# Performance work log

Measured on AMD Instinct MI355X. Metric: run time of the kernel, lower is better.

Reference implementation:

```python
import jax, jax.numpy as jnp
import numpy as np
import math

D_MODEL = 512
NUM_HEADS = 8
D_HEAD = D_MODEL // NUM_HEADS
B, S = 8, 1024


def _rel_shift(pos_score):
    # pos_score: [B, H, S, S] -> Transformer-XL relative shift
    b, h, s1, s2 = pos_score.shape
    padded = jnp.concatenate([jnp.zeros((b, h, s1, 1), pos_score.dtype), pos_score], axis=-1)
    padded = padded.reshape(b, h, s2 + 1, s1)
    return padded[:, :, 1:].reshape(b, h, s1, s2)


def setup_inputs() -> dict:
    key = jax.random.key(0)
    ks = jax.random.split(key, 16)
    scale = 1.0 / math.sqrt(D_MODEL)
    inp = {
        'query': jax.random.normal(ks[0], (B, S, D_MODEL), jnp.float32),
        'key': jax.random.normal(ks[1], (B, S, D_MODEL), jnp.float32),
        'value': jax.random.normal(ks[2], (B, S, D_MODEL), jnp.float32),
        'position_emb': jax.random.normal(ks[3], (B, S, D_MODEL), jnp.float32),
        'Wq': jax.random.normal(ks[4], (D_MODEL, D_MODEL), jnp.float32) * scale,
        'bq': jnp.zeros((D_MODEL,), jnp.float32),
        'Wk': jax.random.normal(ks[5], (D_MODEL, D_MODEL), jnp.float32) * scale,
        'bk': jnp.zeros((D_MODEL,), jnp.float32),
        'Wv': jax.random.normal(ks[6], (D_MODEL, D_MODEL), jnp.float32) * scale,
        'bv': jnp.zeros((D_MODEL,), jnp.float32),
        'Wp': jax.random.normal(ks[7], (D_MODEL, D_MODEL), jnp.float32) * scale,
        'u_bias': jax.random.normal(ks[8], (NUM_HEADS, D_HEAD), jnp.float32) * 0.1,
        'v_bias': jax.random.normal(ks[9], (NUM_HEADS, D_HEAD), jnp.float32) * 0.1,
        'Wo': jax.random.normal(ks[10], (D_MODEL, D_MODEL), jnp.float32) * scale,
        'bo': jnp.zeros((D_MODEL,), jnp.float32),
    }
    return inp


def reference(query, key, value, position_emb, Wq, bq, Wk, bk, Wv, bv, Wp, u_bias, v_bias, Wo, bo):
    b, s, _ = query.shape
    q = (query @ Wq + bq).reshape(b, s, NUM_HEADS, D_HEAD)       # [B,S,H,Dh]
    k = (key @ Wk + bk).reshape(b, s, NUM_HEADS, D_HEAD)
    v = (value @ Wv + bv).reshape(b, s, NUM_HEADS, D_HEAD)
    p = (position_emb @ Wp).reshape(b, s, NUM_HEADS, D_HEAD)
    # content score: (q + u) k^T ; pos score: (q + v) p^T with relative shift
    content_score = jnp.einsum('bqhd,bkhd->bhqk', q + u_bias, k)
    pos_score = _rel_shift(jnp.einsum('bqhd,bkhd->bhqk', q + v_bias, p))
    score = (content_score + pos_score) / math.sqrt(D_MODEL)
    atten = jax.nn.softmax(score, axis=-1)                        # dropout off (eval)
    context = jnp.einsum('bhqk,bkhd->bqhd', atten, v).reshape(b, s, D_MODEL)
    return context @ Wo + bo
```

## Files before the change

kernel.cpp:

```cpp
#include <hip/hip_runtime.h>
#include <cstdint>

typedef unsigned short ushort_t;
typedef __attribute__((ext_vector_type(8))) short bf16x8;
typedef __attribute__((ext_vector_type(4))) float f32x4;

#define S_LEN 1024
#define DHEAD 64

__device__ inline ushort_t f2bf(float f) {
    union { float f; uint32_t u; } c; c.f = f;
    uint32_t u = c.u;
    uint32_t r = u + 0x7FFFu + ((u >> 16) & 1u);
    return (ushort_t)(r >> 16);
}
__device__ inline float bf2f(ushort_t h) {
    union { uint32_t u; float f; } c; c.u = ((uint32_t)h) << 16;
    return c.f;
}
__device__ inline bf16x8 load8(const ushort_t* p) {
    union { uint4 u; bf16x8 v; } c;
    c.u = *reinterpret_cast<const uint4*>(p);
    return c.v;
}

__global__ void prep_kernel(const float* __restrict__ wq, const float* __restrict__ wk,
                            const float* __restrict__ wv, const float* __restrict__ wp,
                            const float* __restrict__ wo, ushort_t* __restrict__ ws) {
    int t = blockIdx.x * 256 + threadIdx.x;
    int wi = blockIdx.y;
    const float* src = wi == 0 ? wq : wi == 1 ? wk : wi == 2 ? wv : wi == 3 ? wp : wo;
    int r = t >> 9, c = t & 511;
    ws[(size_t)wi * 262144 + (size_t)c * 512 + r] = f2bf(src[t]);
}

__global__ __launch_bounds__(256) void proj_gemm(
    const float* __restrict__ qa, const float* __restrict__ ka,
    const float* __restrict__ va, const float* __restrict__ pa,
    const ushort_t* __restrict__ wT,
    const float* __restrict__ bq, const float* __restrict__ bk,
    const float* __restrict__ bv,
    const float* __restrict__ ub, const float* __restrict__ vb,
    ushort_t* __restrict__ Qu, ushort_t* __restrict__ Qv,
    ushort_t* __restrict__ Kp, ushort_t* __restrict__ Pp,
    ushort_t* __restrict__ Vt) {
    __shared__ ushort_t As[128][72];
    __shared__ ushort_t Bs[128][72];
    int z = blockIdx.z;
    const float* A = z == 0 ? qa : z == 1 ? ka : z == 2 ? pa : va;
    const ushort_t* Bt = wT + (z == 0 ? 0 : z == 1 ? 262144 : z == 2 ? 786432 : 524288);
    const float* bias = z == 0 ? bq : z == 1 ? bk : z == 3 ? bv : nullptr;

    int tid = threadIdx.x;
    int wid = tid >> 6, lane = tid & 63, quad = lane >> 4, l16 = lane & 15;
    int wr = wid >> 1, wc = wid & 1;
    int row0 = blockIdx.y * 128, col0 = blockIdx.x * 128;

    f32x4 acc[4][4];
#pragma unroll
    for (int i = 0; i < 4; i++)
#pragma unroll
        for (int j = 0; j < 4; j++) acc[i][j] = (f32x4){0.f, 0.f, 0.f, 0.f};

    for (int k0 = 0; k0 < 512; k0 += 64) {
#pragma unroll
        for (int i = 0; i < 4; i++) {
            int cid = tid + i * 256;
            int r = cid >> 3, c8 = cid & 7;
            const float* ap = A + (size_t)(row0 + r) * 512 + k0 + c8 * 8;
            float4 f0 = *reinterpret_cast<const float4*>(ap);
            float4 f1 = *reinterpret_cast<const float4*>(ap + 4);
            union { ushort_t s[8]; uint4 u; } pk;
            pk.s[0] = f2bf(f0.x); pk.s[1] = f2bf(f0.y); pk.s[2] = f2bf(f0.z); pk.s[3] = f2bf(f0.w);
            pk.s[4] = f2bf(f1.x); pk.s[5] = f2bf(f1.y); pk.s[6] = f2bf(f1.z); pk.s[7] = f2bf(f1.w);
            *reinterpret_cast<uint4*>(&As[r][c8 * 8]) = pk.u;
            *reinterpret_cast<uint4*>(&Bs[r][c8 * 8]) =
                *reinterpret_cast<const uint4*>(Bt + (size_t)(col0 + r) * 512 + k0 + c8 * 8);
        }
        __syncthreads();
#pragma unroll
        for (int kc = 0; kc < 2; kc++) {
            bf16x8 af[4], bg[4];
#pragma unroll
            for (int m = 0; m < 4; m++)
                af[m] = load8(&As[wr * 64 + m * 16 + l16][kc * 32 + quad * 8]);
#pragma unroll
            for (int n = 0; n < 4; n++)
                bg[n] = load8(&Bs[wc * 64 + n * 16 + l16][kc * 32 + quad * 8]);
#pragma unroll
            for (int m = 0; m < 4; m++)
#pragma unroll
                for (int n = 0; n < 4; n++)
                    acc[m][n] = __builtin_amdgcn_mfma_f32_16x16x32_bf16(af[m], bg[n], acc[m][n], 0, 0, 0);
        }
        __syncthreads();
    }

#pragma unroll
    for (int m = 0; m < 4; m++) {
#pragma unroll
        for (int n = 0; n < 4; n++) {
            int col = col0 + wc * 64 + n * 16 + l16;
            float bcol = bias ? bias[col] : 0.f;
#pragma unroll
            for (int r = 0; r < 4; r++) {
                int row = row0 + wr * 64 + m * 16 + quad * 4 + r;
                float val = acc[m][n][r] + bcol;
                int b_ = row >> 10, s_ = row & 1023, h_ = col >> 6, d_ = col & 63;
                if (z == 0) {
                    size_t idx = (((size_t)(b_ * 8 + h_)) * 1024 + s_) * 64 + d_;
                    Qu[idx] = f2bf(val + ub[col]);
                    Qv[idx] = f2bf(val + vb[col]);
                } else if (z == 3) {
                    size_t idx = (((size_t)(b_ * 8 + h_)) * 64 + d_) * 1024 + s_;
                    Vt[idx] = f2bf(val);
                } else {
                    size_t idx = (((size_t)(b_ * 8 + h_)) * 1024 + s_) * 64 + d_;
                    (z == 1 ? Kp : Pp)[idx] = f2bf(val);
                }
            }
        }
    }
}

__global__ __launch_bounds__(256) void out_gemm(
    const ushort_t* __restrict__ A, const ushort_t* __restrict__ Bt,
    const float* __restrict__ bias, float* __restrict__ outf) {
    __shared__ ushort_t As[128][72];
    __shared__ ushort_t Bs[128][72];
    int tid = threadIdx.x;
    int wid = tid >> 6, lane = tid & 63, quad = lane >> 4, l16 = lane & 15;
    int wr = wid >> 1, wc = wid & 1;
    int row0 = blockIdx.y * 128, col0 = blockIdx.x * 128;

    f32x4 acc[4][4];
#pragma unroll
    for (int i = 0; i < 4; i++)
#pragma unroll
        for (int j = 0; j < 4; j++) acc[i][j] = (f32x4){0.f, 0.f, 0.f, 0.f};

    for (int k0 = 0; k0 < 512; k0 += 64) {
#pragma unroll
        for (int i = 0; i < 4; i++) {
            int cid = tid + i * 256;
            int r = cid >> 3, c8 = cid & 7;
            *reinterpret_cast<uint4*>(&As[r][c8 * 8]) =
                *reinterpret_cast<const uint4*>(A + (size_t)(row0 + r) * 512 + k0 + c8 * 8);
            *reinterpret_cast<uint4*>(&Bs[r][c8 * 8]) =
                *reinterpret_cast<const uint4*>(Bt + (size_t)(col0 + r) * 512 + k0 + c8 * 8);
        }
        __syncthreads();
#pragma unroll
        for (int kc = 0; kc < 2; kc++) {
            bf16x8 af[4], bg[4];
#pragma unroll
            for (int m = 0; m < 4; m++)
                af[m] = load8(&As[wr * 64 + m * 16 + l16][kc * 32 + quad * 8]);
#pragma unroll
            for (int n = 0; n < 4; n++)
                bg[n] = load8(&Bs[wc * 64 + n * 16 + l16][kc * 32 + quad * 8]);
#pragma unroll
            for (int m = 0; m < 4; m++)
#pragma unroll
                for (int n = 0; n < 4; n++)
                    acc[m][n] = __builtin_amdgcn_mfma_f32_16x16x32_bf16(af[m], bg[n], acc[m][n], 0, 0, 0);
        }
        __syncthreads();
    }
#pragma unroll
    for (int m = 0; m < 4; m++)
#pragma unroll
        for (int n = 0; n < 4; n++) {
            int col = col0 + wc * 64 + n * 16 + l16;
#pragma unroll
            for (int r = 0; r < 4; r++) {
                int row = row0 + wr * 64 + m * 16 + quad * 4 + r;
                outf[(size_t)row * 512 + col] = acc[m][n][r] + bias[col];
            }
        }
}

__global__ __launch_bounds__(256) void attn_kernel(
    const ushort_t* __restrict__ Qu, const ushort_t* __restrict__ Qv,
    const ushort_t* __restrict__ Kp, const ushort_t* __restrict__ Pp,
    const ushort_t* __restrict__ Vt, ushort_t* __restrict__ ctxb) {
    __shared__ ushort_t sc[16][1032];
    __shared__ float red1[4][16];
    __shared__ float red2[4][16];

    constexpr float SCL = (float)(1.4426950408889634 / 22.627416997969522);

    int bx = blockIdx.x;
    int bh = bx >> 6, q0 = (bx & 63) << 4;
    int tid = threadIdx.x, wid = tid >> 6, lane = tid & 63;
    int quad = lane >> 4, l16 = lane & 15;

    const ushort_t* Qu_b = Qu + (size_t)bh * S_LEN * DHEAD;
    const ushort_t* Qv_b = Qv + (size_t)bh * S_LEN * DHEAD;
    const ushort_t* K_b  = Kp + (size_t)bh * S_LEN * DHEAD;
    const ushort_t* P_b  = Pp + (size_t)bh * S_LEN * DHEAD;
    const ushort_t* V_b  = Vt + (size_t)bh * DHEAD * S_LEN;

    bf16x8 au[2], av1[2], av2[2];
#pragma unroll
    for (int kc = 0; kc < 2; kc++) {
        au[kc]  = load8(Qu_b + (size_t)(q0 + l16) * 64 + kc * 32 + quad * 8);
        av1[kc] = load8(Qv_b + (size_t)(q0 + l16) * 64 + kc * 32 + quad * 8);
        int r2 = q0 + 1 + l16; if (r2 > S_LEN - 1) r2 = S_LEN - 1;
        av2[kc] = load8(Qv_b + (size_t)r2 * 64 + kc * 32 + quad * 8);
    }

    int kw0 = wid << 8, kw1 = kw0 + 256;

    if (lane < 16) {
        int kz = q0 + lane + 1;
        if (kz >= kw0 && kz < kw1) sc[lane][kz] = 0;
    }

    if (kw0 <= q0 + 15) {
        int wlo = (S_LEN - 16) - q0 + kw0;
        int d1 = kw1 - 1 - q0; if (d1 > 0) d1 = 0;
        int whi = (S_LEN - 1) + d1;
        for (int wt = wlo; wt <= whi; wt += 16) {
            int prow = wt + l16; if (prow > S_LEN - 1) prow = S_LEN - 1;
            bf16x8 b0 = load8(P_b + (size_t)prow * 64 + quad * 8);
            bf16x8 b1 = load8(P_b + (size_t)prow * 64 + 32 + quad * 8);
            f32x4 acc = (f32x4){0.f, 0.f, 0.f, 0.f};
            acc = __builtin_amdgcn_mfma_f32_16x16x32_bf16(av1[0], b0, acc, 0, 0, 0);
            acc = __builtin_amdgcn_mfma_f32_16x16x32_bf16(av1[1], b1, acc, 0, 0, 0);
#pragma unroll
            for (int r = 0; r < 4; r++) {
                int m = quad * 4 + r, q = q0 + m;
                int k = wt + l16 - (S_LEN - 1) + q;
                if (k >= kw0 && k < kw1 && k <= q) sc[m][k] = f2bf(acc[r]);
            }
        }
    }
    if (kw1 - 1 >= q0 + 2) {
        int wlo2 = kw0 - q0 - 17; if (wlo2 < 0) wlo2 = 0;
        int whi2 = kw1 - 3 - q0;
        for (int wt = wlo2; wt <= whi2; wt += 16) {
            int prow = wt + l16; if (prow > S_LEN - 1) prow = S_LEN - 1;
            bf16x8 b0 = load8(P_b + (size_t)prow * 64 + quad * 8);
            bf16x8 b1 = load8(P_b + (size_t)prow * 64 + 32 + quad * 8);
            f32x4 acc = (f32x4){0.f, 0.f, 0.f, 0.f};
            acc = __builtin_amdgcn_mfma_f32_16x16x32_bf16(av2[0], b0, acc, 0, 0, 0);
            acc = __builtin_amdgcn_mfma_f32_16x16x32_bf16(av2[1], b1, acc, 0, 0, 0);
#pragma unroll
            for (int r = 0; r < 4; r++) {
                int m = quad * 4 + r, q = q0 + m;
                int k = wt + l16 + q + 2;
                if (k >= kw0 && k < kw1) sc[m][k] = f2bf(acc[r]);
            }
        }
    }

    float pm[4] = {-1e30f, -1e30f, -1e30f, -1e30f};
    for (int nt = 0; nt < 16; ++nt) {
        int kt = kw0 + nt * 16;
        bf16x8 b0 = load8(K_b + (size_t)(kt + l16) * 64 + quad * 8);
        bf16x8 b1 = load8(K_b + (size_t)(kt + l16) * 64 + 32 + quad * 8);
        f32x4 acc;
#pragma unroll
        for (int r = 0; r < 4; r++) acc[r] = bf2f(sc[quad * 4 + r][kt + l16]);
        acc = __builtin_amdgcn_mfma_f32_16x16x32_bf16(au[0], b0, acc, 0, 0, 0);
        acc = __builtin_amdgcn_mfma_f32_16x16x32_bf16(au[1], b1, acc, 0, 0, 0);
#pragma unroll
        for (int r = 0; r < 4; r++) {
            sc[quad * 4 + r][kt + l16] = f2bf(acc[r]);
            pm[r] = fmaxf(pm[r], acc[r]);
        }
    }
#pragma unroll
    for (int off = 1; off < 16; off <<= 1)
#pragma unroll
        for (int r = 0; r < 4; r++) pm[r] = fmaxf(pm[r], __shfl_xor(pm[r], off));
    if (l16 == 0) {
#pragma unroll
        for (int r = 0; r < 4; r++) red1[wid][quad * 4 + r] = pm[r];
    }
    __syncthreads();

    int row = tid & 15, cb = tid >> 4;
    float rm = fmaxf(fmaxf(red1[0][row], red1[1][row]), fmaxf(red1[2][row], red1[3][row]));
    float ssum = 0.f;
    ushort_t* sp = &sc[row][cb * 64];
#pragma unroll
    for (int j = 0; j < 8; j++) {
        union { uint4 u; ushort_t s[8]; } in, out;
        in.u = *reinterpret_cast<uint4*>(sp + j * 8);
#pragma unroll
        for (int e = 0; e < 8; e++) {
            float ev = exp2f((bf2f(in.s[e]) - rm) * SCL);
            out.s[e] = f2bf(ev);
            ssum += ev;
        }
        *reinterpret_cast<uint4*>(sp + j * 8) = out.u;
    }
    ssum += __shfl_xor(ssum, 16);
    ssum += __shfl_xor(ssum, 32);
    if (lane < 16) red2[wid][lane] = ssum;
    __syncthreads();

    int d0 = wid << 4;
    f32x4 acc = (f32x4){0.f, 0.f, 0.f, 0.f};
    for (int kc = 0; kc < 32; ++kc) {
        bf16x8 a = load8(&sc[l16][kc * 32 + quad * 8]);
        bf16x8 b = load8(V_b + (size_t)(d0 + l16) * 1024 + kc * 32 + quad * 8);
        acc = __builtin_amdgcn_mfma_f32_16x16x32_bf16(a, b, acc, 0, 0, 0);
    }
    int b_ = bh >> 3, h_ = bh & 7;
#pragma unroll
    for (int r = 0; r < 4; r++) {
        int m = quad * 4 + r, q = q0 + m;
        float s = red2[0][m] + red2[1][m] + red2[2][m] + red2[3][m];
        ctxb[((size_t)b_ * 1024 + q) * 512 + h_ * 64 + d0 + l16] = f2bf(acc[r] / s);
    }
}

extern "C" void kernel_launch(void* const* d_in, const int* in_sizes, int n_in,
                              void* d_out, int out_size, void* d_ws, size_t ws_size,
                              hipStream_t stream) {
    const float* q  = (const float*)d_in[0];
    const float* k  = (const float*)d_in[1];
    const float* v  = (const float*)d_in[2];
    const float* pe = (const float*)d_in[3];
    const float* Wq = (const float*)d_in[4];
    const float* bq = (const float*)d_in[5];
    const float* Wk = (const float*)d_in[6];
    const float* bk = (const float*)d_in[7];
    const float* Wv = (const float*)d_in[8];
    const float* bv = (const float*)d_in[9];
    const float* Wp = (const float*)d_in[10];
    const float* ub = (const float*)d_in[11];
    const float* vbias = (const float*)d_in[12];
    const float* Wo = (const float*)d_in[13];
    const float* bo = (const float*)d_in[14];
    float* out = (float*)d_out;
    ushort_t* ws = (ushort_t*)d_ws;

    ushort_t* wT  = ws;
    ushort_t* Qu  = ws + 1310720;
    ushort_t* Qv  = Qu + 4194304;
    ushort_t* Kp  = Qv + 4194304;
    ushort_t* Pp  = Kp + 4194304;
    ushort_t* Vt  = Pp + 4194304;
    ushort_t* ctx = Vt + 4194304;

    prep_kernel<<<dim3(1024, 5), 256, 0, stream>>>(Wq, Wk, Wv, Wp, Wo, wT);
    proj_gemm<<<dim3(4, 64, 4), 256, 0, stream>>>(q, k, v, pe, wT, bq, bk, bv,
                                                  ub, vbias, Qu, Qv, Kp, Pp, Vt);
    attn_kernel<<<4096, 256, 0, stream>>>(Qu, Qv, Kp, Pp, Vt, ctx);
    out_gemm<<<dim3(4, 64), 256, 0, stream>>>(ctx, wT + 4 * 262144, bo, out);
}
```

Before: 382.6 us.

## Double query tile in attention, coalesce V transpose and weight prep, prefetch loads

The attention kernel now handles 32 query rows per block instead of 16, so each K and V tile load feeds two MFMA row tiles, and the grid shrinks to half as many blocks. K, P and V fragments are software-prefetched one iteration ahead, and the softmax normalisation uses precomputed reciprocals. Separately, the V projection epilogue stages its output through shared memory so the transposed Vt writes are coalesced, and the weight prep kernel uses a tiled shared-memory transpose. The larger score buffer (about 66KB LDS) may reduce occupancy.

```diff
diff --git a/kernel.cpp b/kernel.cpp
--- a/kernel.cpp
+++ b/kernel.cpp
@@ -24,14 +24,34 @@
     return c.v;
 }
 
-__global__ void prep_kernel(const float* __restrict__ wq, const float* __restrict__ wk,
-                            const float* __restrict__ wv, const float* __restrict__ wp,
-                            const float* __restrict__ wo, ushort_t* __restrict__ ws) {
-    int t = blockIdx.x * 256 + threadIdx.x;
-    int wi = blockIdx.y;
+__global__ __launch_bounds__(256) void prep_kernel(
+    const float* __restrict__ wq, const float* __restrict__ wk,
+    const float* __restrict__ wv, const float* __restrict__ wp,
+    const float* __restrict__ wo, ushort_t* __restrict__ ws) {
+    __shared__ float tile[64][65];
+    int wi = blockIdx.z;
     const float* src = wi == 0 ? wq : wi == 1 ? wk : wi == 2 ? wv : wi == 3 ? wp : wo;
-    int r = t >> 9, c = t & 511;
-    ws[(size_t)wi * 262144 + (size_t)c * 512 + r] = f2bf(src[t]);
+    int cx = blockIdx.x * 64;
+    int ry = blockIdx.y * 64;
+    int t = threadIdx.x;
+    int tr = t >> 4;
+    int tc = (t & 15) * 4;
+#pragma unroll
+    for (int i = 0; i < 4; i++) {
+        int r = tr + i * 16;
+        float4 f = *reinterpret_cast<const float4*>(src + (size_t)(ry + r) * 512 + cx + tc);
+        tile[r][tc] = f.x; tile[r][tc + 1] = f.y; tile[r][tc + 2] = f.z; tile[r][tc + 3] = f.w;
+    }
+    __syncthreads();
+    ushort_t* dst = ws + (size_t)wi * 262144;
+#pragma unroll
+    for (int i = 0; i < 4; i++) {
+        int r = tr + i * 16;
+        ushort4 o;
+        o.x = f2bf(tile[tc][r]); o.y = f2bf(tile[tc + 1][r]);
+        o.z = f2bf(tile[tc + 2][r]); o.w = f2bf(tile[tc + 3][r]);
+        *reinterpret_cast<ushort4*>(dst + (size_t)(cx + r) * 512 + ry + tc) = o;
+    }
 }
 
 __global__ __launch_bounds__(256) void proj_gemm(
@@ -44,8 +64,7 @@
     ushort_t* __restrict__ Qu, ushort_t* __restrict__ Qv,
     ushort_t* __restrict__ Kp, ushort_t* __restrict__ Pp,
     ushort_t* __restrict__ Vt) {
-    __shared__ ushort_t As[128][72];
-    __shared__ ushort_t Bs[128][72];
+    __shared__ ushort_t smem[2][128][72];
     int z = blockIdx.z;
     const float* A = z == 0 ? qa : z == 1 ? ka : z == 2 ? pa : va;
     const ushort_t* Bt = wT + (z == 0 ? 0 : z == 1 ? 262144 : z == 2 ? 786432 : 524288);
@@ -73,8 +92,8 @@
             union { ushort_t s[8]; uint4 u; } pk;
             pk.s[0] = f2bf(f0.x); pk.s[1] = f2bf(f0.y); pk.s[2] = f2bf(f0.z); pk.s[3] = f2bf(f0.w);
             pk.s[4] = f2bf(f1.x); pk.s[5] = f2bf(f1.y); pk.s[6] = f2bf(f1.z); pk.s[7] = f2bf(f1.w);
-            *reinterpret_cast<uint4*>(&As[r][c8 * 8]) = pk.u;
-            *reinterpret_cast<uint4*>(&Bs[r][c8 * 8]) =
+            *reinterpret_cast<uint4*>(&smem[0][r][c8 * 8]) = pk.u;
+            *reinterpret_cast<uint4*>(&smem[1][r][c8 * 8]) =
                 *reinterpret_cast<const uint4*>(Bt + (size_t)(col0 + r) * 512 + k0 + c8 * 8);
         }
         __syncthreads();
@@ -83,10 +102,10 @@
             bf16x8 af[4], bg[4];
 #pragma unroll
             for (int m = 0; m < 4; m++)
-                af[m] = load8(&As[wr * 64 + m * 16 + l16][kc * 32 + quad * 8]);
+                af[m] = load8(&smem[0][wr * 64 + m * 16 + l16][kc * 32 + quad * 8]);
 #pragma unroll
             for (int n = 0; n < 4; n++)
-                bg[n] = load8(&Bs[wc * 64 + n * 16 + l16][kc * 32 + quad * 8]);
+                bg[n] = load8(&smem[1][wc * 64 + n * 16 + l16][kc * 32 + quad * 8]);
 #pragma unroll
             for (int m = 0; m < 4; m++)
 #pragma unroll
@@ -96,30 +115,54 @@
         __syncthreads();
     }
 
-#pragma unroll
-    for (int m = 0; m < 4; m++) {
-#pragma unroll
-        for (int n = 0; n < 4; n++) {
-            int col = col0 + wc * 64 + n * 16 + l16;
-            float bcol = bias ? bias[col] : 0.f;
-#pragma unroll
-            for (int r = 0; r < 4; r++) {
-                int row = row0 + wr * 64 + m * 16 + quad * 4 + r;
-                float val = acc[m][n][r] + bcol;
-                int b_ = row >> 10, s_ = row & 1023, h_ = col >> 6, d_ = col & 63;
-                if (z == 0) {
+    if (z == 3) {
+        ushort_t (*Ts)[130] = reinterpret_cast<ushort_t(*)[130]>(&smem[0][0][0]);
+#pragma unroll
+        for (int m = 0; m < 4; m++)
+#pragma unroll
+            for (int n = 0; n < 4; n++) {
+                int dl = wc * 64 + n * 16 + l16;
+                float bcol = bv[col0 + dl];
+#pragma unroll
+                for (int r = 0; r < 4; r++) {
+                    int sl = wr * 64 + m * 16 + quad * 4 + r;
+                    Ts[dl][sl] = f2bf(acc[m][n][r] + bcol);
+                }
+            }
+        __syncthreads();
+        int b_ = row0 >> 10, s0 = row0 & 1023;
+#pragma unroll
+        for (int p = 0; p < 8; p++) {
+            int dl = p * 16 + (tid >> 4);
+            int sl = (tid & 15) * 8;
+            int col = col0 + dl, h_ = col >> 6, d_ = col & 63;
+            ushort_t* dst = Vt + (((size_t)(b_ * 8 + h_)) * 64 + d_) * 1024 + s0 + sl;
+            union { uint4 u; ushort_t s[8]; } pk;
+#pragma unroll
+            for (int e = 0; e < 8; e++) pk.s[e] = Ts[dl][sl + e];
+            *reinterpret_cast<uint4*>(dst) = pk.u;
+        }
+    } else {
+#pragma unroll
+        for (int m = 0; m < 4; m++)
+#pragma unroll
+            for (int n = 0; n < 4; n++) {
+                int col = col0 + wc * 64 + n * 16 + l16;
+                float bcol = bias ? bias[col] : 0.f;
+#pragma unroll
+                for (int r = 0; r < 4; r++) {
+                    int row = row0 + wr * 64 + m * 16 + quad * 4 + r;
+                    float val = acc[m][n][r] + bcol;
+                    int b_ = row >> 10, s_ = row & 1023, h_ = col >> 6, d_ = col & 63;
                     size_t idx = (((size_t)(b_ * 8 + h_)) * 1024 + s_) * 64 + d_;
-                    Qu[idx] = f2bf(val + ub[col]);
-                    Qv[idx] = f2bf(val + vb[col]);
-                } else if (z == 3) {
-                    size_t idx = (((size_t)(b_ * 8 + h_)) * 64 + d_) * 1024 + s_;
-                    Vt[idx] = f2bf(val);
-                } else {
-                    size_t idx = (((size_t)(b_ * 8 + h_)) * 1024 + s_) * 64 + d_;
-                    (z == 1 ? Kp : Pp)[idx] = f2bf(val);
+                    if (z == 0) {
+                        Qu[idx] = f2bf(val + ub[col]);
+                        Qv[idx] = f2bf(val + vb[col]);
+                    } else {
+                        (z == 1 ? Kp : Pp)[idx] = f2bf(val);
+                    }
                 }
             }
-        }
     }
 }
 
@@ -184,14 +227,15 @@
     const ushort_t* __restrict__ Qu, const ushort_t* __restrict__ Qv,
     const ushort_t* __restrict__ Kp, const ushort_t* __restrict__ Pp,
     const ushort_t* __restrict__ Vt, ushort_t* __restrict__ ctxb) {
-    __shared__ ushort_t sc[16][1032];
-    __shared__ float red1[4][16];
-    __shared__ float red2[4][16];
+    __shared__ ushort_t sc[32][1032];
+    __shared__ float red1[4][32];
+    __shared__ float red2[32][8];
+    __shared__ float rowinv[32];
 
     constexpr float SCL = (float)(1.4426950408889634 / 22.627416997969522);
 
     int bx = blockIdx.x;
-    int bh = bx >> 6, q0 = (bx & 63) << 4;
+    int bh = bx >> 5, q0 = (bx & 31) << 5;
     int tid = threadIdx.x, wid = tid >> 6, lane = tid & 63;
     int quad = lane >> 4, l16 = lane & 15;
 
@@ -201,92 +245,134 @@
     const ushort_t* P_b  = Pp + (size_t)bh * S_LEN * DHEAD;
     const ushort_t* V_b  = Vt + (size_t)bh * DHEAD * S_LEN;
 
-    bf16x8 au[2], av1[2], av2[2];
+    int kw0 = wid << 8, kw1 = kw0 + 256;
+
+    bf16x8 au0[2], au1[2];
 #pragma unroll
     for (int kc = 0; kc < 2; kc++) {
-        au[kc]  = load8(Qu_b + (size_t)(q0 + l16) * 64 + kc * 32 + quad * 8);
-        av1[kc] = load8(Qv_b + (size_t)(q0 + l16) * 64 + kc * 32 + quad * 8);
-        int r2 = q0 + 1 + l16; if (r2 > S_LEN - 1) r2 = S_LEN - 1;
-        av2[kc] = load8(Qv_b + (size_t)r2 * 64 + kc * 32 + quad * 8);
-    }
-
-    int kw0 = wid << 8, kw1 = kw0 + 256;
-
-    if (lane < 16) {
+        au0[kc] = load8(Qu_b + (size_t)(q0 + l16) * 64 + kc * 32 + quad * 8);
+        au1[kc] = load8(Qu_b + (size_t)(q0 + 16 + l16) * 64 + kc * 32 + quad * 8);
+    }
+
+    if (lane < 32) {
         int kz = q0 + lane + 1;
         if (kz >= kw0 && kz < kw1) sc[lane][kz] = 0;
     }
 
-    if (kw0 <= q0 + 15) {
-        int wlo = (S_LEN - 16) - q0 + kw0;
-        int d1 = kw1 - 1 - q0; if (d1 > 0) d1 = 0;
-        int whi = (S_LEN - 1) + d1;
-        for (int wt = wlo; wt <= whi; wt += 16) {
-            int prow = wt + l16; if (prow > S_LEN - 1) prow = S_LEN - 1;
-            bf16x8 b0 = load8(P_b + (size_t)prow * 64 + quad * 8);
-            bf16x8 b1 = load8(P_b + (size_t)prow * 64 + 32 + quad * 8);
-            f32x4 acc = (f32x4){0.f, 0.f, 0.f, 0.f};
-            acc = __builtin_amdgcn_mfma_f32_16x16x32_bf16(av1[0], b0, acc, 0, 0, 0);
-            acc = __builtin_amdgcn_mfma_f32_16x16x32_bf16(av1[1], b1, acc, 0, 0, 0);
-#pragma unroll
-            for (int r = 0; r < 4; r++) {
-                int m = quad * 4 + r, q = q0 + m;
-                int k = wt + l16 - (S_LEN - 1) + q;
-                if (k >= kw0 && k < kw1 && k <= q) sc[m][k] = f2bf(acc[r]);
+#pragma unroll
+    for (int mt = 0; mt < 2; mt++) {
+        int q0m = q0 + mt * 16;
+        bf16x8 av1[2], av2[2];
+#pragma unroll
+        for (int kc = 0; kc < 2; kc++) {
+            av1[kc] = load8(Qv_b + (size_t)(q0m + l16) * 64 + kc * 32 + quad * 8);
+            int r2 = q0m + 1 + l16; if (r2 > S_LEN - 1) r2 = S_LEN - 1;
+            av2[kc] = load8(Qv_b + (size_t)r2 * 64 + kc * 32 + quad * 8);
+        }
+        if (kw0 <= q0m + 15) {
+            int wlo = (S_LEN - 16) - q0m + kw0;
+            int d1 = kw1 - 1 - q0m; if (d1 > 0) d1 = 0;
+            int whi = (S_LEN - 1) + d1;
+            int pr = wlo + l16; if (pr > S_LEN - 1) pr = S_LEN - 1;
+            bf16x8 p0 = load8(P_b + (size_t)pr * 64 + quad * 8);
+            bf16x8 p1 = load8(P_b + (size_t)pr * 64 + 32 + quad * 8);
+            for (int wt = wlo; wt <= whi; wt += 16) {
+                bf16x8 b0 = p0, b1 = p1;
+                if (wt + 16 <= whi) {
+                    int pn = wt + 16 + l16; if (pn > S_LEN - 1) pn = S_LEN - 1;
+                    p0 = load8(P_b + (size_t)pn * 64 + quad * 8);
+                    p1 = load8(P_b + (size_t)pn * 64 + 32 + quad * 8);
+                }
+                f32x4 acc = (f32x4){0.f, 0.f, 0.f, 0.f};
+                acc = __builtin_amdgcn_mfma_f32_16x16x32_bf16(av1[0], b0, acc, 0, 0, 0);
+                acc = __builtin_amdgcn_mfma_f32_16x16x32_bf16(av1[1], b1, acc, 0, 0, 0);
+#pragma unroll
+                for (int r = 0; r < 4; r++) {
+                    int m = quad * 4 + r, q = q0m + m;
+                    int k = wt + l16 - (S_LEN - 1) + q;
+                    if (k >= kw0 && k < kw1 && k <= q) sc[mt * 16 + m][k] = f2bf(acc[r]);
+                }
             }
         }
-    }
-    if (kw1 - 1 >= q0 + 2) {
-        int wlo2 = kw0 - q0 - 17; if (wlo2 < 0) wlo2 = 0;
-        int whi2 = kw1 - 3 - q0;
-        for (int wt = wlo2; wt <= whi2; wt += 16) {
-            int prow = wt + l16; if (prow > S_LEN - 1) prow = S_LEN - 1;
-            bf16x8 b0 = load8(P_b + (size_t)prow * 64 + quad * 8);
-            bf16x8 b1 = load8(P_b + (size_t)prow * 64 + 32 + quad * 8);
-            f32x4 acc = (f32x4){0.f, 0.f, 0.f, 0.f};
-            acc = __builtin_amdgcn_mfma_f32_16x16x32_bf16(av2[0], b0, acc, 0, 0, 0);
-            acc = __builtin_amdgcn_mfma_f32_16x16x32_bf16(av2[1], b1, acc, 0, 0, 0);
-#pragma unroll
-            for (int r = 0; r < 4; r++) {
-                int m = quad * 4 + r, q = q0 + m;
-                int k = wt + l16 + q + 2;
-                if (k >= kw0 && k < kw1) sc[m][k] = f2bf(acc[r]);
+        if (kw1 - 1 >= q0m + 2) {
+            int wlo2 = kw0 - q0m - 17; if (wlo2 < 0) wlo2 = 0;
+            int whi2 = kw1 - 3 - q0m;
+            int pr = wlo2 + l16; if (pr > S_LEN - 1) pr = S_LEN - 1;
+            bf16x8 p0 = load8(P_b + (size_t)pr * 64 + quad * 8);
+            bf16x8 p1 = load8(P_b + (size_t)pr * 64 + 32 + quad * 8);
+            for (int wt = wlo2; wt <= whi2; wt += 16) {
+                bf16x8 b0 = p0, b1 = p1;
+                if (wt + 16 <= whi2) {
+                    int pn = wt + 16 + l16; if (pn > S_LEN - 1) pn = S_LEN - 1;
+                    p0 = load8(P_b + (size_t)pn * 64 + quad * 8);
+                    p1 = load8(P_b + (size_t)pn * 64 + 32 + quad * 8);
+                }
+                f32x4 acc = (f32x4){0.f, 0.f, 0.f, 0.f};
+                acc = __builtin_amdgcn_mfma_f32_16x16x32_bf16(av2[0], b0, acc, 0, 0, 0);
+                acc = __builtin_amdgcn_mfma_f32_16x16x32_bf16(av2[1], b1, acc, 0, 0, 0);
+#pragma unroll
+                for (int r = 0; r < 4; r++) {
+                    int m = quad * 4 + r, q = q0m + m;
+                    int k = wt + l16 + q + 2;
+                    if (k >= kw0 && k < kw1) sc[mt * 16 + m][k] = f2bf(acc[r]);
+                }
             }
         }
     }
 
-    float pm[4] = {-1e30f, -1e30f, -1e30f, -1e30f};
+    float pm0[4] = {-1e30f, -1e30f, -1e30f, -1e30f};
+    float pm1[4] = {-1e30f, -1e30f, -1e30f, -1e30f};
+    const ushort_t* Kw = K_b + (size_t)kw0 * 64;
+    bf16x8 k0 = load8(Kw + (size_t)l16 * 64 + quad * 8);
+    bf16x8 k1 = load8(Kw + (size_t)l16 * 64 + 32 + quad * 8);
     for (int nt = 0; nt < 16; ++nt) {
         int kt = kw0 + nt * 16;
-        bf16x8 b0 = load8(K_b + (size_t)(kt + l16) * 64 + quad * 8);
-        bf16x8 b1 = load8(K_b + (size_t)(kt + l16) * 64 + 32 + quad * 8);
-        f32x4 acc;
-#pragma unroll
-        for (int r = 0; r < 4; r++) acc[r] = bf2f(sc[quad * 4 + r][kt + l16]);
-        acc = __builtin_amdgcn_mfma_f32_16x16x32_bf16(au[0], b0, acc, 0, 0, 0);
-        acc = __builtin_amdgcn_mfma_f32_16x16x32_bf16(au[1], b1, acc, 0, 0, 0);
+        bf16x8 b0 = k0, b1 = k1;
+        if (nt < 15) {
+            const ushort_t* kp = Kw + (size_t)((nt + 1) * 16 + l16) * 64;
+            k0 = load8(kp + quad * 8);
+            k1 = load8(kp + 32 + quad * 8);
+        }
+        f32x4 a0, a1;
 #pragma unroll
         for (int r = 0; r < 4; r++) {
-            sc[quad * 4 + r][kt + l16] = f2bf(acc[r]);
-            pm[r] = fmaxf(pm[r], acc[r]);
+            a0[r] = bf2f(sc[quad * 4 + r][kt + l16]);
+            a1[r] = bf2f(sc[16 + quad * 4 + r][kt + l16]);
+        }
+        a0 = __builtin_amdgcn_mfma_f32_16x16x32_bf16(au0[0], b0, a0, 0, 0, 0);
+        a0 = __builtin_amdgcn_mfma_f32_16x16x32_bf16(au0[1], b1, a0, 0, 0, 0);
+        a1 = __builtin_amdgcn_mfma_f32_16x16x32_bf16(au1[0], b0, a1, 0, 0, 0);
+        a1 = __builtin_amdgcn_mfma_f32_16x16x32_bf16(au1[1], b1, a1, 0, 0, 0);
+#pragma unroll
+        for (int r = 0; r < 4; r++) {
+            sc[quad * 4 + r][kt + l16] = f2bf(a0[r]);
+            sc[16 + quad * 4 + r][kt + l16] = f2bf(a1[r]);
+            pm0[r] = fmaxf(pm0[r], a0[r]);
+            pm1[r] = fmaxf(pm1[r], a1[r]);
         }
     }
 #pragma unroll
     for (int off = 1; off < 16; off <<= 1)
 #pragma unroll
-        for (int r = 0; r < 4; r++) pm[r] = fmaxf(pm[r], __shfl_xor(pm[r], off));
+        for (int r = 0; r < 4; r++) {
+            pm0[r] = fmaxf(pm0[r], __shfl_xor(pm0[r], off));
+            pm1[r] = fmaxf(pm1[r], __shfl_xor(pm1[r], off));
+        }
     if (l16 == 0) {
 #pragma unroll
-        for (int r = 0; r < 4; r++) red1[wid][quad * 4 + r] = pm[r];
+        for (int r = 0; r < 4; r++) {
+            red1[wid][quad * 4 + r] = pm0[r];
+            red1[wid][16 + quad * 4 + r] = pm1[r];
+        }
     }
     __syncthreads();
 
-    int row = tid & 15, cb = tid >> 4;
+    int row = tid & 31, cb = tid >> 5;
     float rm = fmaxf(fmaxf(red1[0][row], red1[1][row]), fmaxf(red1[2][row], red1[3][row]));
     float ssum = 0.f;
-    ushort_t* sp = &sc[row][cb * 64];
-#pragma unroll
-    for (int j = 0; j < 8; j++) {
+    ushort_t* sp = &sc[row][cb * 128];
+#pragma unroll
+    for (int j = 0; j < 16; j++) {
         union { uint4 u; ushort_t s[8]; } in, out;
         in.u = *reinterpret_cast<uint4*>(sp + j * 8);
 #pragma unroll
@@ -297,24 +383,37 @@
         }
         *reinterpret_cast<uint4*>(sp + j * 8) = out.u;
     }
-    ssum += __shfl_xor(ssum, 16);
-    ssum += __shfl_xor(ssum, 32);
-    if (lane < 16) red2[wid][lane] = ssum;
+    red2[row][cb] = ssum;
     __syncthreads();
+    if (tid < 32) {
+        float s = 0.f;
+#pragma unroll
+        for (int c = 0; c < 8; c++) s += red2[tid][c];
+        rowinv[tid] = 1.0f / s;
+    }
 
     int d0 = wid << 4;
-    f32x4 acc = (f32x4){0.f, 0.f, 0.f, 0.f};
+    const ushort_t* Vw = V_b + (size_t)(d0 + l16) * 1024;
+    bf16x8 vb0 = load8(Vw + quad * 8);
+    f32x4 ac0 = (f32x4){0.f, 0.f, 0.f, 0.f};
+    f32x4 ac1 = (f32x4){0.f, 0.f, 0.f, 0.f};
     for (int kc = 0; kc < 32; ++kc) {
-        bf16x8 a = load8(&sc[l16][kc * 32 + quad * 8]);
-        bf16x8 b = load8(V_b + (size_t)(d0 + l16) * 1024 + kc * 32 + quad * 8);
-        acc = __builtin_amdgcn_mfma_f32_16x16x32_bf16(a, b, acc, 0, 0, 0);
-    }
+        bf16x8 b = vb0;
+        if (kc < 31) vb0 = load8(Vw + (kc + 1) * 32 + quad * 8);
+        bf16x8 a0 = load8(&sc[l16][kc * 32 + quad * 8]);
+        bf16x8 a1 = load8(&sc[16 + l16][kc * 32 + quad * 8]);
+        ac0 = __builtin_amdgcn_mfma_f32_16x16x32_bf16(a0, b, ac0, 0, 0, 0);
+        ac1 = __builtin_amdgcn_mfma_f32_16x16x32_bf16(a1, b, ac1, 0, 0, 0);
+    }
+    __syncthreads();
     int b_ = bh >> 3, h_ = bh & 7;
 #pragma unroll
     for (int r = 0; r < 4; r++) {
-        int m = quad * 4 + r, q = q0 + m;
-        float s = red2[0][m] + red2[1][m] + red2[2][m] + red2[3][m];
-        ctxb[((size_t)b_ * 1024 + q) * 512 + h_ * 64 + d0 + l16] = f2bf(acc[r] / s);
+        int m = quad * 4 + r;
+        ctxb[((size_t)b_ * 1024 + (q0 + m)) * 512 + h_ * 64 + d0 + l16] =
+            f2bf(ac0[r] * rowinv[m]);
+        ctxb[((size_t)b_ * 1024 + (q0 + 16 + m)) * 512 + h_ * 64 + d0 + l16] =
+            f2bf(ac1[r] * rowinv[16 + m]);
     }
 }
 
@@ -347,9 +446,9 @@
     ushort_t* Vt  = Pp + 4194304;
     ushort_t* ctx = Vt + 4194304;
 
-    prep_kernel<<<dim3(1024, 5), 256, 0, stream>>>(Wq, Wk, Wv, Wp, Wo, wT);
+    prep_kernel<<<dim3(8, 8, 5), 256, 0, stream>>>(Wq, Wk, Wv, Wp, Wo, wT);
     proj_gemm<<<dim3(4, 64, 4), 256, 0, stream>>>(q, k, v, pe, wT, bq, bk, bv,
                                                   ub, vbias, Qu, Qv, Kp, Pp, Vt);
-    attn_kernel<<<4096, 256, 0, stream>>>(Qu, Qv, Kp, Pp, Vt, ctx);
+    attn_kernel<<<2048, 256, 0, stream>>>(Qu, Qv, Kp, Pp, Vt, ctx);
     out_gemm<<<dim3(4, 64), 256, 0, stream>>>(ctx, wT + 4 * 262144, bo, out);
 }
```

New measurement: 337.4 us. 1.13x faster.
